# Optimization experiments

Hardware: AMD Instinct MI355X
Metric: run time of the kernel (lower is better)

The kernel has to match this reference:

```python
import jax, jax.numpy as jnp
import numpy as np

IN_CH = 256
HID = 32
OUT_CH = 32
EPS = 1e-5


def setup_inputs() -> dict:
    key = jax.random.key(0)
    ks = jax.random.split(key, 7)
    B, L = 1, 256
    x = jax.random.normal(ks[0], (B, L, IN_CH), dtype=jnp.float32)
    # nn.Linear(in_channels, hidden_dim)
    W1 = jax.random.normal(ks[1], (IN_CH, HID), dtype=jnp.float32) / np.sqrt(IN_CH)
    b1 = jnp.zeros((HID,), dtype=jnp.float32)
    # nn.LayerNorm(hidden_dim * hidden_dim)
    gamma = jnp.ones((HID * HID,), dtype=jnp.float32)
    beta = jnp.zeros((HID * HID,), dtype=jnp.float32)
    # nn.Linear(hidden_dim * hidden_dim, out_channels)
    W2 = jax.random.normal(ks[2], (HID * HID, OUT_CH), dtype=jnp.float32) / np.sqrt(HID * HID)
    b2 = jnp.zeros((OUT_CH,), dtype=jnp.float32)
    return {"x": x, "W1": W1, "b1": b1, "gamma": gamma, "beta": beta, "W2": W2, "b2": b2}


def reference(x, W1, b1, gamma, beta, W2, b2):
    # a: [B, L, HID]
    a = jnp.einsum('bic,ch->bih', x, W1) + b1
    # outer product: [B, I, J, D, E] -> flatten to [B, I, J, D*E]
    outer = jnp.einsum('bid,bje->bijde', a, a)
    B, I, J, D, E = outer.shape
    outer = outer.reshape(B, I, J, D * E)
    # LayerNorm over last dim
    mu = jnp.mean(outer, axis=-1, keepdims=True)
    var = jnp.mean(jnp.square(outer - mu), axis=-1, keepdims=True)
    normed = (outer - mu) * jax.lax.rsqrt(var + EPS) * gamma + beta
    # final projection: [B, I, J, OUT_CH]
    return jnp.einsum('bijk,ko->bijo', normed, W2) + b2
```

## Files before the change

kernel.cpp:

```cpp
#include <hip/hip_runtime.h>

#define LSEQ 256
#define INC  256
#define HID  32
#define OUTC 32
#define DE   1024
#define EPSV 1e-5f

#define ASTR 264
#define TSTR 36

__global__ __launch_bounds__(256) void k1_aT(
    const float* __restrict__ x, const float* __restrict__ W1, const float* __restrict__ b1,
    const float* __restrict__ gamma, const float* __restrict__ beta,
    const float* __restrict__ W2, const float* __restrict__ b2,
    float* __restrict__ a, float* __restrict__ S, float* __restrict__ Q,
    float* __restrict__ T, float* __restrict__ GW, float* __restrict__ C)
{
    __shared__ float sh[256];
    __shared__ float sh2[256];
    __shared__ float xL[256];
    __shared__ float aL[32];
    const int t = threadIdx.x;
    const int b = blockIdx.x;

    if (b < 256) {
        const int j = b;
        xL[t] = x[j * INC + t];
        __syncthreads();

        const int d = t & 31, kc = t >> 5;
        const float* w = W1 + (kc * 32) * HID + d;
        float p0 = 0.f, p1 = 0.f;
        #pragma unroll
        for (int k = 0; k < 16; ++k) {
            p0 = fmaf(xL[kc * 32 + 2 * k],     w[(2 * k) * HID],     p0);
            p1 = fmaf(xL[kc * 32 + 2 * k + 1], w[(2 * k + 1) * HID], p1);
        }
        sh[t] = p0 + p1;
        __syncthreads();

        if (t < 32) {
            float tot = b1[t];
            #pragma unroll
            for (int c = 0; c < 8; ++c) tot += sh[c * 32 + t];
            aL[t] = tot;
            a[j * HID + t] = tot;
            float s = tot, q = tot * tot;
            #pragma unroll
            for (int off = 16; off > 0; off >>= 1) {
                s += __shfl_xor(s, off);
                q += __shfl_xor(q, off);
            }
            if (t == 0) { S[j] = s; Q[j] = q; }
        }
        __syncthreads();

        const int dd = t >> 3, o4 = (t & 7) * 4;
        float4 acc = {0.f, 0.f, 0.f, 0.f};
        #pragma unroll
        for (int e = 0; e < 32; ++e) {
            const float g = gamma[dd * 32 + e] * aL[e];
            const float4 wv = *(const float4*)(W2 + (dd * 32 + e) * OUTC + o4);
            acc.x = fmaf(g, wv.x, acc.x);
            acc.y = fmaf(g, wv.y, acc.y);
            acc.z = fmaf(g, wv.z, acc.z);
            acc.w = fmaf(g, wv.w, acc.w);
        }
        *(float4*)(T + j * DE + dd * 32 + o4) = acc;
    } else {
        const int o = t & 31, chunk = t >> 5;
        float gw = 0.f, bw = 0.f;
        for (int k = 0; k < 128; ++k) {
            const int de = chunk * 128 + k;
            const float w = W2[de * OUTC + o];
            gw = fmaf(gamma[de], w, gw);
            bw = fmaf(beta[de],  w, bw);
        }
        sh[t] = gw; sh2[t] = bw;
        __syncthreads();
        if (t < 32) {
            float g = 0.f, bb = 0.f;
            #pragma unroll
            for (int c2 = 0; c2 < 8; ++c2) { g += sh[c2 * 32 + t]; bb += sh2[c2 * 32 + t]; }
            GW[t] = g;
            C[t]  = bb + b2[t];
        }
    }
}

__global__ __launch_bounds__(256) void k2_gemm(
    const float* __restrict__ a, const float* __restrict__ S, const float* __restrict__ Q,
    const float* __restrict__ GW, const float* __restrict__ C,
    const float* __restrict__ T, float* __restrict__ out)
{
    const int bid = blockIdx.x;
    const int j = bid & 255, half = bid >> 8;
    const int t = threadIdx.x;
    __shared__ float aPad[16 * ASTR];
    __shared__ float tPad[32 * TSTR];
    __shared__ float sL[LSEQ];
    __shared__ float qL[LSEQ];
    __shared__ float gwL[OUTC], cL[OUTC];

    {
        const int r = t >> 1, p = t & 1;
        const float4* ar4 = (const float4*)(a + (half * 128 + r) * HID + p * 16);
        const int base = (r >> 3) * ASTR + (r & 7);
        #pragma unroll
        for (int c = 0; c < 4; ++c) {
            const float4 v = ar4[c];
            const int dd = p * 16 + c * 4;
            aPad[base + (dd + 0) * 8] = v.x;
            aPad[base + (dd + 1) * 8] = v.y;
            aPad[base + (dd + 2) * 8] = v.z;
            aPad[base + (dd + 3) * 8] = v.w;
        }
    }
    {
        const float4 v = *(const float4*)(T + j * DE + t * 4);
        const int dd = t >> 3, o4 = (t & 7) * 4;
        *(float4*)(tPad + dd * TSTR + o4) = v;
    }
    sL[t] = S[t];
    qL[t] = Q[t];
    if (t < OUTC) { gwL[t] = GW[t]; cL[t] = C[t]; }
    __syncthreads();

    const int iT = t >> 3, oT = t & 7;
    const int abase = (iT >> 1) * ASTR + (iT & 1) * 4;
    float acc[4][4];
    #pragma unroll
    for (int m = 0; m < 4; ++m)
        #pragma unroll
        for (int k = 0; k < 4; ++k) acc[m][k] = 0.f;

    #pragma unroll
    for (int d = 0; d < 32; ++d) {
        const float4 av = *(const float4*)(aPad + abase + d * 8);
        const float4 tv = *(const float4*)(tPad + d * TSTR + oT * 4);
        const float am[4] = {av.x, av.y, av.z, av.w};
        const float tk[4] = {tv.x, tv.y, tv.z, tv.w};
        #pragma unroll
        for (int m = 0; m < 4; ++m)
            #pragma unroll
            for (int k = 0; k < 4; ++k)
                acc[m][k] = fmaf(am[m], tk[k], acc[m][k]);
    }

    const float Sj = sL[j], Qj = qL[j];
    const float gw0 = gwL[oT * 4 + 0], gw1 = gwL[oT * 4 + 1];
    const float gw2 = gwL[oT * 4 + 2], gw3 = gwL[oT * 4 + 3];
    const float c0 = cL[oT * 4 + 0], c1 = cL[oT * 4 + 1];
    const float c2 = cL[oT * 4 + 2], c3 = cL[oT * 4 + 3];

    #pragma unroll
    for (int m = 0; m < 4; ++m) {
        const int lr = (iT >> 1) * 8 + (iT & 1) * 4 + m;
        const int i = half * 128 + lr;
        const float Si = sL[i], Qi = qL[i];
        const float mu  = Si * Sj * (1.0f / 1024.0f);
        const float ex2 = Qi * Qj * (1.0f / 1024.0f);
        const float var = ex2 - mu * mu;
        const float r   = rsqrtf(var + EPSV);
        float4 o4v;
        o4v.x = fmaf(r, acc[m][0] - mu * gw0, c0);
        o4v.y = fmaf(r, acc[m][1] - mu * gw1, c1);
        o4v.z = fmaf(r, acc[m][2] - mu * gw2, c2);
        o4v.w = fmaf(r, acc[m][3] - mu * gw3, c3);
        *(float4*)(out + (i * LSEQ + j) * OUTC + oT * 4) = o4v;
    }
}

extern "C" void kernel_launch(void* const* d_in, const int* in_sizes, int n_in,
                              void* d_out, int out_size, void* d_ws, size_t ws_size,
                              hipStream_t stream)
{
    const float* x     = (const float*)d_in[0];
    const float* W1    = (const float*)d_in[1];
    const float* b1    = (const float*)d_in[2];
    const float* gamma = (const float*)d_in[3];
    const float* beta  = (const float*)d_in[4];
    const float* W2    = (const float*)d_in[5];
    const float* b2    = (const float*)d_in[6];
    float* out = (float*)d_out;

    float* ws = (float*)d_ws;
    float* a  = ws;
    float* S  = ws + 8192;
    float* Q  = ws + 8448;
    float* GW = ws + 8704;
    float* C  = ws + 8736;
    float* T  = ws + 8768;

    k1_aT<<<257, 256, 0, stream>>>(x, W1, b1, gamma, beta, W2, b2, a, S, Q, T, GW, C);
    k2_gemm<<<512, 256, 0, stream>>>(a, S, Q, GW, C, T, out);
}
```

Measured before the change: 77.57 us.

## Fuse both stages into one cooperative kernel with grid sync

Merges the two-kernel pipeline into a single cooperative launch of 256 blocks. Each block computes its row of a, its T slice and a redundant gamma/beta·W2 reduction, then stashes a/S/Q in the output buffer and grid-syncs. After that, every block reads all of a and computes 256 rows of output per j, with 8x4 register tiles. This removes the second launch and the workspace round trip, at the cost of two grid-wide barriers, fewer and larger blocks, more shared memory and register pressure, and redundant per-block GW/C computation.

```diff
diff --git a/kernel.cpp b/kernel.cpp
--- a/kernel.cpp
+++ b/kernel.cpp
@@ -1,4 +1,7 @@
 #include <hip/hip_runtime.h>
+#include <hip/hip_cooperative_groups.h>
+
+namespace cg = cooperative_groups;
 
 #define LSEQ 256
 #define INC  256
@@ -10,25 +13,34 @@
 #define ASTR 264
 #define TSTR 36
 
-__global__ __launch_bounds__(256) void k1_aT(
+__global__ __launch_bounds__(256) void fused_opm(
     const float* __restrict__ x, const float* __restrict__ W1, const float* __restrict__ b1,
     const float* __restrict__ gamma, const float* __restrict__ beta,
     const float* __restrict__ W2, const float* __restrict__ b2,
-    float* __restrict__ a, float* __restrict__ S, float* __restrict__ Q,
-    float* __restrict__ T, float* __restrict__ GW, float* __restrict__ C)
+    float* out)
 {
+    const int j = blockIdx.x;
+    const int t = threadIdx.x;
+
+    __shared__ float xL[INC];
     __shared__ float sh[256];
-    __shared__ float sh2[256];
-    __shared__ float xL[256];
-    __shared__ float aL[32];
-    const int t = threadIdx.x;
-    const int b = blockIdx.x;
+    __shared__ float aL[HID];
+    __shared__ float tPad[HID * TSTR];
+    __shared__ float redG[HID * TSTR];
+    __shared__ float redB[HID * TSTR];
+    __shared__ float gwL[OUTC], cL[OUTC];
+    __shared__ float aPad[32 * ASTR];
+    __shared__ float sL[LSEQ];
+    __shared__ float qL[LSEQ];
 
-    if (b < 256) {
-        const int j = b;
-        xL[t] = x[j * INC + t];
-        __syncthreads();
+    float* stash_a = out;
+    float* stash_S = out + 8192;
+    float* stash_Q = out + 8448;
 
+    xL[t] = x[j * INC + t];
+    __syncthreads();
+
+    {
         const int d = t & 31, kc = t >> 5;
         const float* w = W1 + (kc * 32) * HID + d;
         float p0 = 0.f, p1 = 0.f;
@@ -38,111 +50,104 @@
             p1 = fmaf(xL[kc * 32 + 2 * k + 1], w[(2 * k + 1) * HID], p1);
         }
         sh[t] = p0 + p1;
-        __syncthreads();
+    }
+    __syncthreads();
 
-        if (t < 32) {
-            float tot = b1[t];
-            #pragma unroll
-            for (int c = 0; c < 8; ++c) tot += sh[c * 32 + t];
-            aL[t] = tot;
-            a[j * HID + t] = tot;
-            float s = tot, q = tot * tot;
-            #pragma unroll
-            for (int off = 16; off > 0; off >>= 1) {
-                s += __shfl_xor(s, off);
-                q += __shfl_xor(q, off);
-            }
-            if (t == 0) { S[j] = s; Q[j] = q; }
+    if (t < 32) {
+        float tot = b1[t];
+        #pragma unroll
+        for (int c = 0; c < 8; ++c) tot += sh[c * 32 + t];
+        aL[t] = tot;
+        stash_a[j * HID + t] = tot;
+        float s = tot, q = tot * tot;
+        #pragma unroll
+        for (int off = 16; off > 0; off >>= 1) {
+            s += __shfl_xor(s, off);
+            q += __shfl_xor(q, off);
         }
-        __syncthreads();
+        if (t == 0) { stash_S[j] = s; stash_Q[j] = q; }
+    }
+    __syncthreads();
 
+    {
         const int dd = t >> 3, o4 = (t & 7) * 4;
-        float4 acc = {0.f, 0.f, 0.f, 0.f};
+        float4 tAcc = {0.f, 0.f, 0.f, 0.f};
+        float4 gAcc = {0.f, 0.f, 0.f, 0.f};
+        float4 bAcc = {0.f, 0.f, 0.f, 0.f};
         #pragma unroll
         for (int e = 0; e < 32; ++e) {
-            const float g = gamma[dd * 32 + e] * aL[e];
-            const float4 wv = *(const float4*)(W2 + (dd * 32 + e) * OUTC + o4);
-            acc.x = fmaf(g, wv.x, acc.x);
-            acc.y = fmaf(g, wv.y, acc.y);
-            acc.z = fmaf(g, wv.z, acc.z);
-            acc.w = fmaf(g, wv.w, acc.w);
+            const int de = dd * 32 + e;
+            const float g  = gamma[de];
+            const float bb = beta[de];
+            const float ga = g * aL[e];
+            const float4 w4 = *(const float4*)(W2 + de * OUTC + o4);
+            tAcc.x = fmaf(ga, w4.x, tAcc.x);
+            tAcc.y = fmaf(ga, w4.y, tAcc.y);
+            tAcc.z = fmaf(ga, w4.z, tAcc.z);
+            tAcc.w = fmaf(ga, w4.w, tAcc.w);
+            gAcc.x = fmaf(g,  w4.x, gAcc.x);
+            gAcc.y = fmaf(g,  w4.y, gAcc.y);
+            gAcc.z = fmaf(g,  w4.z, gAcc.z);
+            gAcc.w = fmaf(g,  w4.w, gAcc.w);
+            bAcc.x = fmaf(bb, w4.x, bAcc.x);
+            bAcc.y = fmaf(bb, w4.y, bAcc.y);
+            bAcc.z = fmaf(bb, w4.z, bAcc.z);
+            bAcc.w = fmaf(bb, w4.w, bAcc.w);
         }
-        *(float4*)(T + j * DE + dd * 32 + o4) = acc;
-    } else {
-        const int o = t & 31, chunk = t >> 5;
-        float gw = 0.f, bw = 0.f;
-        for (int k = 0; k < 128; ++k) {
-            const int de = chunk * 128 + k;
-            const float w = W2[de * OUTC + o];
-            gw = fmaf(gamma[de], w, gw);
-            bw = fmaf(beta[de],  w, bw);
+        *(float4*)(tPad + dd * TSTR + o4) = tAcc;
+        *(float4*)(redG + dd * TSTR + o4) = gAcc;
+        *(float4*)(redB + dd * TSTR + o4) = bAcc;
+    }
+    __syncthreads();
+
+    if (t < 32) {
+        float g = 0.f, bb = 0.f;
+        #pragma unroll
+        for (int dd = 0; dd < 32; ++dd) {
+            g  += redG[dd * TSTR + t];
+            bb += redB[dd * TSTR + t];
         }
-        sh[t] = gw; sh2[t] = bw;
-        __syncthreads();
-        if (t < 32) {
-            float g = 0.f, bb = 0.f;
-            #pragma unroll
-            for (int c2 = 0; c2 < 8; ++c2) { g += sh[c2 * 32 + t]; bb += sh2[c2 * 32 + t]; }
-            GW[t] = g;
-            C[t]  = bb + b2[t];
-        }
+        gwL[t] = g;
+        cL[t]  = bb + b2[t];
     }
-}
 
-__global__ __launch_bounds__(256) void k2_gemm(
-    const float* __restrict__ a, const float* __restrict__ S, const float* __restrict__ Q,
-    const float* __restrict__ GW, const float* __restrict__ C,
-    const float* __restrict__ T, float* __restrict__ out)
-{
-    const int bid = blockIdx.x;
-    const int j = bid & 255, half = bid >> 8;
-    const int t = threadIdx.x;
-    __shared__ float aPad[16 * ASTR];
-    __shared__ float tPad[32 * TSTR];
-    __shared__ float sL[LSEQ];
-    __shared__ float qL[LSEQ];
-    __shared__ float gwL[OUTC], cL[OUTC];
+    __threadfence();
+    cg::this_grid().sync();
 
     {
-        const int r = t >> 1, p = t & 1;
-        const float4* ar4 = (const float4*)(a + (half * 128 + r) * HID + p * 16);
-        const int base = (r >> 3) * ASTR + (r & 7);
+        const float4* ar4 = (const float4*)(stash_a + t * HID);
+        const int base = (t >> 3) * ASTR + (t & 7);
         #pragma unroll
-        for (int c = 0; c < 4; ++c) {
+        for (int c = 0; c < 8; ++c) {
             const float4 v = ar4[c];
-            const int dd = p * 16 + c * 4;
-            aPad[base + (dd + 0) * 8] = v.x;
-            aPad[base + (dd + 1) * 8] = v.y;
-            aPad[base + (dd + 2) * 8] = v.z;
-            aPad[base + (dd + 3) * 8] = v.w;
+            const int d = c * 4;
+            aPad[base + (d + 0) * 8] = v.x;
+            aPad[base + (d + 1) * 8] = v.y;
+            aPad[base + (d + 2) * 8] = v.z;
+            aPad[base + (d + 3) * 8] = v.w;
         }
+        sL[t] = stash_S[t];
+        qL[t] = stash_Q[t];
     }
-    {
-        const float4 v = *(const float4*)(T + j * DE + t * 4);
-        const int dd = t >> 3, o4 = (t & 7) * 4;
-        *(float4*)(tPad + dd * TSTR + o4) = v;
-    }
-    sL[t] = S[t];
-    qL[t] = Q[t];
-    if (t < OUTC) { gwL[t] = GW[t]; cL[t] = C[t]; }
-    __syncthreads();
+    cg::this_grid().sync();
 
     const int iT = t >> 3, oT = t & 7;
-    const int abase = (iT >> 1) * ASTR + (iT & 1) * 4;
-    float acc[4][4];
+    const int abase = iT * ASTR;
+    float acc[8][4];
     #pragma unroll
-    for (int m = 0; m < 4; ++m)
+    for (int m = 0; m < 8; ++m)
         #pragma unroll
         for (int k = 0; k < 4; ++k) acc[m][k] = 0.f;
 
     #pragma unroll
     for (int d = 0; d < 32; ++d) {
-        const float4 av = *(const float4*)(aPad + abase + d * 8);
-        const float4 tv = *(const float4*)(tPad + d * TSTR + oT * 4);
-        const float am[4] = {av.x, av.y, av.z, av.w};
-        const float tk[4] = {tv.x, tv.y, tv.z, tv.w};
+        const float4 a0 = *(const float4*)(aPad + abase + d * 8);
+        const float4 a1 = *(const float4*)(aPad + abase + d * 8 + 4);
+        const float4 tf = *(const float4*)(tPad + d * TSTR + oT * 4);
+        const float am[8] = {a0.x, a0.y, a0.z, a0.w, a1.x, a1.y, a1.z, a1.w};
+        const float tk[4] = {tf.x, tf.y, tf.z, tf.w};
         #pragma unroll
-        for (int m = 0; m < 4; ++m)
+        for (int m = 0; m < 8; ++m)
             #pragma unroll
             for (int k = 0; k < 4; ++k)
                 acc[m][k] = fmaf(am[m], tk[k], acc[m][k]);
@@ -155,9 +160,8 @@
     const float c2 = cL[oT * 4 + 2], c3 = cL[oT * 4 + 3];
 
     #pragma unroll
-    for (int m = 0; m < 4; ++m) {
-        const int lr = (iT >> 1) * 8 + (iT & 1) * 4 + m;
-        const int i = half * 128 + lr;
+    for (int m = 0; m < 8; ++m) {
+        const int i = iT * 8 + m;
         const float Si = sL[i], Qi = qL[i];
         const float mu  = Si * Sj * (1.0f / 1024.0f);
         const float ex2 = Qi * Qj * (1.0f / 1024.0f);
@@ -184,15 +188,10 @@
     const float* W2    = (const float*)d_in[5];
     const float* b2    = (const float*)d_in[6];
     float* out = (float*)d_out;
+    (void)d_ws; (void)ws_size;
 
-    float* ws = (float*)d_ws;
-    float* a  = ws;
-    float* S  = ws + 8192;
-    float* Q  = ws + 8448;
-    float* GW = ws + 8704;
-    float* C  = ws + 8736;
-    float* T  = ws + 8768;
-
-    k1_aT<<<257, 256, 0, stream>>>(x, W1, b1, gamma, beta, W2, b2, a, S, Q, T, GW, C);
-    k2_gemm<<<512, 256, 0, stream>>>(a, S, Q, GW, C, T, out);
+    void* args[] = {(void*)&x, (void*)&W1, (void*)&b1, (void*)&gamma,
+                    (void*)&beta, (void*)&W2, (void*)&b2, (void*)&out};
+    hipLaunchCooperativeKernel((const void*)fused_opm,
+                               dim3(LSEQ), dim3(256), args, 0, stream);
 }
```

Result: slower. 159.2 us (+105.2%).
